# Performance work log

Hardware: AMD Instinct MI355X
Metric: run time of the kernel (lower is better)

Reference implementation:

```python
import jax, jax.numpy as jnp
import numpy as np

N_NODES = 100000
N_EDGES = 1600000
N_GRAPHS = 128
D = 64
EPS = 1e-5


def layer_norm(h, gamma, beta):
    mu = jnp.mean(h, axis=-1, keepdims=True)
    var = jnp.var(h, axis=-1, keepdims=True)
    return (h - mu) * jax.lax.rsqrt(var + EPS) * gamma + beta


def setup_inputs() -> dict:
    key = jax.random.key(0)
    ks = jax.random.split(key, 9)
    x = jax.random.normal(ks[0], (N_NODES, D), dtype=jnp.float32)
    edge_index = jax.random.randint(ks[1], (2, N_EDGES), 0, N_NODES, dtype=jnp.int64)
    batch = jnp.sort(jax.random.randint(ks[2], (N_NODES,), 0, N_GRAPHS, dtype=jnp.int64))
    graph_embed = jax.random.normal(ks[3], (N_GRAPHS, D), dtype=jnp.float32)
    s = 1.0 / np.sqrt(D)
    W_self = jax.random.uniform(ks[4], (D, D), jnp.float32, -s, s)
    W_neigh = jax.random.uniform(ks[5], (D, D), jnp.float32, -s, s)
    b = jax.random.uniform(ks[6], (D,), jnp.float32, -s, s)
    gamma = jnp.ones((D,), jnp.float32)
    beta = jnp.zeros((D,), jnp.float32)
    return {"x": x, "edge_index": edge_index, "batch": batch,
            "graph_embed": graph_embed, "W_self": W_self, "W_neigh": W_neigh,
            "b": b, "gamma": gamma, "beta": beta}


def reference(x, edge_index, batch, graph_embed, W_self, W_neigh, b, gamma, beta):
    src, dst = edge_index[0], edge_index[1]
    # mean neighbor aggregation: gather src features, scatter-add into dst
    msg_sum = jax.ops.segment_sum(x[src], dst, num_segments=N_NODES)  # [N, D]
    deg = jax.ops.segment_sum(jnp.ones((N_EDGES,), x.dtype), dst, num_segments=N_NODES)
    h_neigh = msg_sum / jnp.maximum(deg, 1.0)[:, None]
    # SAGEConv combine
    node_out = x @ W_self + h_neigh @ W_neigh + b  # [N, D]
    # graph_aggr='add' pooling over batch assignment
    graph_out = jax.ops.segment_sum(node_out, batch, num_segments=N_GRAPHS)  # [G, D]
    # residual (channel_match=True -> no projection)
    node_out = node_out + x
    graph_out = graph_out + graph_embed
    # norm then act; note: original applies norm TWICE to graph_out and no ReLU on it
    node_out = jax.nn.relu(layer_norm(node_out, gamma, beta))
    graph_out = layer_norm(layer_norm(graph_out, gamma, beta), gamma, beta)
    return (node_out, graph_out)
```

## Files before the change

kernel.cpp:

```cpp
#include <hip/hip_runtime.h>

#define N_NODES  100000
#define N_EDGES  1600000
#define N_GRAPHS 128
#define DD       64
#define EPSV     1e-5f

#define BSH      5
#define BMASK    31
#define NBUCK    3125
#define NBPAD    4096
#define CAPB     768

#define THRP     1024
#define EPT      16
#define BLKE     (THRP*EPT)
#define NBLK     ((N_EDGES + BLKE - 1) / BLKE)

#define O_ORD   200704u
#define O_DESC  6754304u
#define O_GACC  9801216u
#define O_XB    9834496u
#define O_WTF   22634496u
#define WS_NEED (O_WTF + 16384u)

typedef __attribute__((ext_vector_type(8))) short bf16x8;
typedef __attribute__((ext_vector_type(4))) float f32x4;
typedef __attribute__((ext_vector_type(2))) float f32x2;

__device__ __forceinline__ ushort bf16rne(float f) {
  uint u = __float_as_uint(f);
  return (ushort)((u + 0x7FFFu + ((u >> 16) & 1u)) >> 16);
}
__device__ __forceinline__ uint pk2(float lo, float hi) {
  return (uint)bf16rne(lo) | ((uint)bf16rne(hi) << 16);
}

__global__ __launch_bounds__(256) void cast_k(const float* __restrict__ x, ushort* __restrict__ xb,
                                              float* __restrict__ gacc) {
  int i = blockIdx.x * 256 + threadIdx.x;
  if (i < N_GRAPHS * DD) gacc[i] = 0.f;
  if (i < 128) gacc[N_GRAPHS * DD + i] = 0.f;
  float4 v = ((const float4*)x)[i];
  uint4 u = *(const uint4*)&v;
  ushort4 o;
  o.x = (ushort)((u.x + 0x7FFFu + ((u.x >> 16) & 1)) >> 16);
  o.y = (ushort)((u.y + 0x7FFFu + ((u.y >> 16) & 1)) >> 16);
  o.z = (ushort)((u.z + 0x7FFFu + ((u.z >> 16) & 1)) >> 16);
  o.w = (ushort)((u.w + 0x7FFFu + ((u.w >> 16) & 1)) >> 16);
  ((ushort4*)xb)[i] = o;
}

__global__ __launch_bounds__(1024) void scatS_k(const int* __restrict__ ei,
                                                int* __restrict__ ordered,
                                                int* __restrict__ desc,
                                                const float* __restrict__ Wself,
                                                const float* __restrict__ Wneigh,
                                                ushort* __restrict__ wtf) {
  __shared__ int hist[NBPAD];
  __shared__ int cur2[NBPAD];
  __shared__ int wtot[16];
  int t = threadIdx.x;
  if (blockIdx.x == 0) {
    int lane = t & 63, ks = (t >> 6) & 3, tile = (t >> 8) & 1, nt = t >> 9;
    int brow = (nt << 5) + (tile << 4) + (lane & 15);
    int k0 = (ks << 5) + (((lane >> 4) & 3) << 3);
    uint4 o;
    uint p[4];
#pragma unroll
    for (int jj = 0; jj < 4; ++jj) {
      int k = k0 + jj * 2;
      float w0 = (k < 64)     ? Wself[k * DD + brow]       : Wneigh[(k - 64) * DD + brow];
      float w1 = (k + 1 < 64) ? Wself[(k + 1) * DD + brow] : Wneigh[(k - 63) * DD + brow];
      p[jj] = pk2(w0, w1);
    }
    o.x = p[0]; o.y = p[1]; o.z = p[2]; o.w = p[3];
    ((uint4*)wtf)[t] = o;
  }
  for (int i = t; i < NBPAD; i += THRP) hist[i] = 0;
  __syncthreads();
  int e0 = blockIdx.x * BLKE;
  int pk[EPT], bn[EPT];
#pragma unroll
  for (int j = 0; j < EPT; ++j) {
    int e = e0 + j * THRP + t;
    bn[j] = -1;
    if (e < N_EDGES) {
      int s = ei[e], d = ei[N_EDGES + e];
      bn[j] = d >> BSH;
      pk[j] = s | ((d & BMASK) << 17);
      atomicAdd(&hist[bn[j]], 1);
    }
  }
  __syncthreads();
  int h0 = hist[4 * t], h1 = hist[4 * t + 1], h2 = hist[4 * t + 2], h3 = hist[4 * t + 3];
  int s = h0 + h1 + h2 + h3;
  int lane = t & 63, wv = t >> 6;
  int inc = s;
#pragma unroll
  for (int off = 1; off < 64; off <<= 1) {
    int u = __shfl_up(inc, off);
    if (lane >= off) inc += u;
  }
  if (lane == 63) wtot[wv] = inc;
  __syncthreads();
  if (t < 16) {
    int v = wtot[t];
    int iv = v;
#pragma unroll
    for (int off = 1; off < 16; off <<= 1) {
      int u = __shfl_up(iv, off);
      if (t >= off) iv += u;
    }
    wtot[t] = iv - v;
  }
  __syncthreads();
  int base = wtot[wv] + (inc - s);
  cur2[4 * t]     = base;
  cur2[4 * t + 1] = base + h0;
  cur2[4 * t + 2] = base + h0 + h1;
  cur2[4 * t + 3] = base + h0 + h1 + h2;
  {
    int dbase = blockIdx.x * NBUCK;
#pragma unroll
    for (int i = 0; i < 4; ++i) {
      int bb = 4 * t + i;
      if (bb < NBUCK) desc[dbase + bb] = (cur2[bb] << 10) | hist[bb];
    }
  }
  __syncthreads();
  int obase = blockIdx.x * BLKE;
#pragma unroll
  for (int j = 0; j < EPT; ++j) {
    if (bn[j] >= 0) {
      int sp = atomicAdd(&cur2[bn[j]], 1);
      ordered[obase + sp] = pk[j];
    }
  }
}

__global__ __launch_bounds__(256, 8) void aggM_k(const ushort* __restrict__ xb,
                                                 const int* __restrict__ ordered,
                                                 const int* __restrict__ desc,
                                                 const ushort* __restrict__ wtf,
                                                 const float* __restrict__ bvec,
                                                 const float* __restrict__ gamma,
                                                 const float* __restrict__ beta,
                                                 const int* __restrict__ batch,
                                                 float* __restrict__ gacc,
                                                 float* __restrict__ out) {
  __shared__ short As[32 * 128];
  __shared__ float Cbuf[32 * 65];
  __shared__ int sorted[CAPB + 16];
  __shared__ int hist[32], startc[32], curl[32];
  __shared__ int wsum2[2];
  __shared__ int nTot_s;
  int* slabL = (int*)Cbuf;
  int t = threadIdx.x;
  int b = blockIdx.x;
  int node0 = b << BSH;
  if (t < 32) hist[t] = 0;
  {
    uint4 v = ((const uint4*)(xb + (size_t)node0 * DD))[t];
    uint r = (uint)t >> 3, c = (uint)t & 7;
    *(uint4*)((char*)As + r * 256u + ((c * 16u) ^ ((r & 7u) << 4))) = v;
  }
  int dsc = (t < NBLK) ? desc[t * NBUCK + b] : 0;
  int c   = dsc & 1023;
  int st  = dsc >> 10;
  int inc = c;
  if (t < 128) {
    int lane = t & 63;
#pragma unroll
    for (int off = 1; off < 64; off <<= 1) {
      int u = __shfl_up(inc, off);
      if (lane >= off) inc += u;
    }
    if (lane == 63) wsum2[t >> 6] = inc;
  }
  __syncthreads();
  int pos = 0;
  if (t < 128) pos = ((t >> 6) ? wsum2[0] : 0) + inc - c;
  if (t == 0) nTot_s = wsum2[0] + wsum2[1];
  if (t < NBLK) {
    int lim = CAPB - pos;
    int cc = c < lim ? c : (lim > 0 ? lim : 0);
    const int* srcp = ordered + (size_t)t * BLKE + st;
    for (int i = 0; i < cc; ++i) slabL[pos + i] = srcp[i];
  }
  __syncthreads();
  int n = nTot_s;
  if (n > CAPB) n = CAPB;
  int w0 = -1, w1 = -1, w2 = -1;
  if (t < n)       { w0 = slabL[t];       atomicAdd(&hist[w0 >> 17], 1); }
  if (t + 256 < n) { w1 = slabL[t + 256]; atomicAdd(&hist[w1 >> 17], 1); }
  if (t + 512 < n) { w2 = slabL[t + 512]; atomicAdd(&hist[w2 >> 17], 1); }
  __syncthreads();
  if (t < 32) {
    int h = hist[t];
    int v = h;
#pragma unroll
    for (int off = 1; off < 32; off <<= 1) {
      int u = __shfl_up(v, off);
      if (t >= off) v += u;
    }
    startc[t] = v - h;
    curl[t]   = v - h;
  }
  __syncthreads();
  if (w0 >= 0) { int p = atomicAdd(&curl[w0 >> 17], 1); sorted[p] = ((w0 & 0x1FFFF) << 7) + 512; }
  if (w1 >= 0) { int p = atomicAdd(&curl[w1 >> 17], 1); sorted[p] = ((w1 & 0x1FFFF) << 7) + 512; }
  if (w2 >= 0) { int p = atomicAdd(&curl[w2 >> 17], 1); sorted[p] = ((w2 & 0x1FFFF) << 7) + 512; }
  __syncthreads();
  int wl   = __builtin_amdgcn_readfirstlane(t >> 6);
  int lane = t & 63;
  int g    = lane >> 4;
  int sub  = lane & 15;
  const char* zb = (const char*)xb - 512;
  uint subb = (uint)sub * 8u;
  for (int r = wl; r < 32; r += 4) {
    int s0 = startc[r], dg = hist[r];
    f32x2 A01 = {0.f, 0.f}, A23 = {0.f, 0.f};
    for (int j = 0; j < dg; j += 16) {
      int e0 = j + g, e1 = j + 4 + g, e2 = j + 8 + g, e3 = j + 12 + g;
      uint o0 = (uint)sorted[s0 + e0]; if (e0 >= dg) o0 = 0u;
      uint o1 = (uint)sorted[s0 + e1]; if (e1 >= dg) o1 = 0u;
      uint o2 = (uint)sorted[s0 + e2]; if (e2 >= dg) o2 = 0u;
      uint o3 = (uint)sorted[s0 + e3]; if (e3 >= dg) o3 = 0u;
      uint2 u0 = *(const uint2*)(zb + o0 + subb);
      uint2 u1 = *(const uint2*)(zb + o1 + subb);
      uint2 u2 = *(const uint2*)(zb + o2 + subb);
      uint2 u3 = *(const uint2*)(zb + o3 + subb);
      f32x2 v0, v1, v2, v3, y0, y1, y2, y3;
      v0.x = __uint_as_float(u0.x << 16); v0.y = __uint_as_float(u0.x & 0xFFFF0000u);
      v1.x = __uint_as_float(u1.x << 16); v1.y = __uint_as_float(u1.x & 0xFFFF0000u);
      v2.x = __uint_as_float(u2.x << 16); v2.y = __uint_as_float(u2.x & 0xFFFF0000u);
      v3.x = __uint_as_float(u3.x << 16); v3.y = __uint_as_float(u3.x & 0xFFFF0000u);
      y0.x = __uint_as_float(u0.y << 16); y0.y = __uint_as_float(u0.y & 0xFFFF0000u);
      y1.x = __uint_as_float(u1.y << 16); y1.y = __uint_as_float(u1.y & 0xFFFF0000u);
      y2.x = __uint_as_float(u2.y << 16); y2.y = __uint_as_float(u2.y & 0xFFFF0000u);
      y3.x = __uint_as_float(u3.y << 16); y3.y = __uint_as_float(u3.y & 0xFFFF0000u);
      A01 += (v0 + v1) + (v2 + v3);
      A23 += (y0 + y1) + (y2 + y3);
    }
    float a0 = A01.x, a1 = A01.y, a2 = A23.x, a3 = A23.y;
#pragma unroll
    for (int off = 16; off <= 32; off <<= 1) {
      a0 += __shfl_xor(a0, off);
      a1 += __shfl_xor(a1, off);
      a2 += __shfl_xor(a2, off);
      a3 += __shfl_xor(a3, off);
    }
    if (g == 0) {
      float inv = 1.f / fmaxf((float)dg, 1.f);
      uint2 pw;
      pw.x = pk2(a0 * inv, a1 * inv);
      pw.y = pk2(a2 * inv, a3 * inv);
      uint rr = (uint)r;
      *(uint2*)((char*)As + rr * 256u + ((128u + (uint)sub * 8u) ^ ((rr & 7u) << 4))) = pw;
    }
  }
  __syncthreads();
  f32x4 acc0 = {0.f, 0.f, 0.f, 0.f}, acc1 = {0.f, 0.f, 0.f, 0.f};
  uint mrow  = (uint)(wl >> 1) << 4;
  int  nt    = wl & 1;
  uint arow  = mrow + (uint)(lane & 15);
  uint kc    = ((uint)(lane >> 4)) * 16u;
#pragma unroll 1
  for (int ks = 0; ks < 4; ++ks) {
    uint kb = (uint)ks * 64u + kc;
    bf16x8 af = *(const bf16x8*)((const char*)As + arow * 256u + (kb ^ ((arow & 7u) << 4)));
    bf16x8 b0 = *(const bf16x8*)(wtf + (size_t)(((nt * 2 + 0) * 4 + ks) * 64 + lane) * 8);
    bf16x8 b1 = *(const bf16x8*)(wtf + (size_t)(((nt * 2 + 1) * 4 + ks) * 64 + lane) * 8);
    acc0 = __builtin_amdgcn_mfma_f32_16x16x32_bf16(af, b0, acc0, 0, 0, 0);
    acc1 = __builtin_amdgcn_mfma_f32_16x16x32_bf16(af, b1, acc1, 0, 0, 0);
  }
  {
    uint nbase = (uint)nt << 5;
    uint rr = mrow + (((uint)(lane >> 4)) << 2);
    uint cc = nbase + (uint)(lane & 15);
#pragma unroll
    for (int j = 0; j < 4; ++j) {
      uint rj = rr + (uint)j;
      Cbuf[rj * 65u + cc]       = acc0[j];
      Cbuf[rj * 65u + cc + 16u] = acc1[j];
    }
  }
  __syncthreads();
  float bv  = bvec[lane];
  float gv  = gamma[lane];
  float btv = beta[lane];
  int r0 = wl * 8;
  int gprev = -1; float pool = 0.f;
#pragma unroll
  for (int m = 0; m < 8; ++m) {
    uint r = (uint)(r0 + m);
    int node = node0 + r0 + m;
    float cval = Cbuf[r * 65u + (uint)lane];
    float tmp = cval + bv;
    int gi = batch[node];
    if (gi != gprev) {
      if (gprev >= 0) atomicAdd(&gacc[gprev * DD + lane], pool);
      pool = 0.f; gprev = gi;
    }
    pool += tmp;
    ushort xv16 = *(const ushort*)((const char*)As + r * 256u + (((uint)lane * 2u) ^ ((r & 7u) << 4)));
    float val = tmp + __uint_as_float((uint)xv16 << 16);
    float s = val;
    for (int off = 32; off; off >>= 1) s += __shfl_xor(s, off);
    float mu  = s * (1.f / 64.f);
    float dlt = val - mu;
    float ss  = dlt * dlt;
    for (int off = 32; off; off >>= 1) ss += __shfl_xor(ss, off);
    float rstd = rsqrtf(ss * (1.f / 64.f) + EPSV);
    float o = dlt * rstd * gv + btv;
    out[(size_t)node * DD + lane] = fmaxf(o, 0.f);
  }
  if (gprev >= 0) atomicAdd(&gacc[gprev * DD + lane], pool);
}

__global__ __launch_bounds__(256) void graph_k(const float* __restrict__ gacc, const float* __restrict__ gemb,
                                               const float* __restrict__ gamma, const float* __restrict__ beta,
                                               float* __restrict__ out) {
  int lane = threadIdx.x & 63;
  int w = blockIdx.x * 4 + (threadIdx.x >> 6);
  if (w >= N_GRAPHS) return;
  float v = gacc[w * DD + lane] + gemb[w * DD + lane];
  float gv = gamma[lane], btv = beta[lane];
#pragma unroll
  for (int it = 0; it < 2; ++it) {
    float s = v;
    for (int off = 32; off; off >>= 1) s += __shfl_xor(s, off);
    float mu  = s * (1.f / 64.f);
    float d   = v - mu;
    float ss  = d * d;
    for (int off = 32; off; off >>= 1) ss += __shfl_xor(ss, off);
    v = d * rsqrtf(ss * (1.f / 64.f) + EPSV) * gv + btv;
  }
  out[(size_t)N_NODES * DD + w * DD + lane] = v;
}

extern "C" void kernel_launch(void* const* d_in, const int* in_sizes, int n_in,
                              void* d_out, int out_size, void* d_ws, size_t ws_size,
                              hipStream_t stream) {
  const float* x      = (const float*)d_in[0];
  const int*   ei     = (const int*)d_in[1];
  const int*   batch  = (const int*)d_in[2];
  const float* gemb   = (const float*)d_in[3];
  const float* Wself  = (const float*)d_in[4];
  const float* Wneigh = (const float*)d_in[5];
  const float* bvec   = (const float*)d_in[6];
  const float* gamma  = (const float*)d_in[7];
  const float* beta   = (const float*)d_in[8];

  char* ws = (char*)d_ws;
  int*    ordered = (int*)(ws + O_ORD);
  int*    desc    = (int*)(ws + O_DESC);
  float*  gacc    = (float*)(ws + O_GACC);
  ushort* xb      = (ushort*)(ws + O_XB);
  ushort* wtf     = (ushort*)(ws + O_WTF);
  float*  outf    = (float*)d_out;

  cast_k <<<N_NODES * DD / 4 / 256, 256, 0, stream>>>(x, xb, gacc);
  scatS_k<<<NBLK, THRP, 0, stream>>>(ei, ordered, desc, Wself, Wneigh, wtf);
  aggM_k <<<NBUCK, 256, 0, stream>>>(xb, ordered, desc, wtf, bvec, gamma, beta,
                                     batch, gacc, outf);
  graph_k<<<N_GRAPHS / 4, 256, 0, stream>>>(gacc, gemb, gamma, beta, outf);
}
```

Baseline: 89.40 us.

## Transpose bucket descriptors and gather edges by binary search instead of serial copy

After: 87.45 us. 1.02x faster.

```diff
diff --git a/kernel.cpp b/kernel.cpp
--- a/kernel.cpp
+++ b/kernel.cpp
@@ -121,11 +121,10 @@
   cur2[4 * t + 2] = base + h0 + h1;
   cur2[4 * t + 3] = base + h0 + h1 + h2;
   {
-    int dbase = blockIdx.x * NBUCK;
 #pragma unroll
     for (int i = 0; i < 4; ++i) {
       int bb = 4 * t + i;
-      if (bb < NBUCK) desc[dbase + bb] = (cur2[bb] << 10) | hist[bb];
+      if (bb < NBUCK) desc[bb * NBLK + blockIdx.x] = (cur2[bb] << 10) | hist[bb];
     }
   }
   __syncthreads();
@@ -155,7 +154,8 @@
   __shared__ int hist[32], startc[32], curl[32];
   __shared__ int wsum2[2];
   __shared__ int nTot_s;
-  int* slabL = (int*)Cbuf;
+  int* posA = sorted;
+  int* stA  = sorted + 128;
   int t = threadIdx.x;
   int b = blockIdx.x;
   int node0 = b << BSH;
@@ -165,7 +165,7 @@
     uint r = (uint)t >> 3, c = (uint)t & 7;
     *(uint4*)((char*)As + r * 256u + ((c * 16u) ^ ((r & 7u) << 4))) = v;
   }
-  int dsc = (t < NBLK) ? desc[t * NBUCK + b] : 0;
+  int dsc = (t < NBLK) ? desc[b * NBLK + t] : 0;
   int c   = dsc & 1023;
   int st  = dsc >> 10;
   int inc = c;
@@ -179,22 +179,28 @@
     if (lane == 63) wsum2[t >> 6] = inc;
   }
   __syncthreads();
-  int pos = 0;
-  if (t < 128) pos = ((t >> 6) ? wsum2[0] : 0) + inc - c;
+  if (t < 128) {
+    int pos = ((t >> 6) ? wsum2[0] : 0) + inc - c;
+    posA[t] = (t < NBLK) ? pos : 0x7FFFFFFF;
+    stA[t]  = t * BLKE + st;
+  }
   if (t == 0) nTot_s = wsum2[0] + wsum2[1];
-  if (t < NBLK) {
-    int lim = CAPB - pos;
-    int cc = c < lim ? c : (lim > 0 ? lim : 0);
-    const int* srcp = ordered + (size_t)t * BLKE + st;
-    for (int i = 0; i < cc; ++i) slabL[pos + i] = srcp[i];
-  }
   __syncthreads();
   int n = nTot_s;
   if (n > CAPB) n = CAPB;
+  auto bs_load = [&](int i) -> int {
+    int lo = 0;
+#pragma unroll
+    for (int stp = 64; stp; stp >>= 1) {
+      int cnd = lo + stp;
+      lo = (posA[cnd] <= i) ? cnd : lo;
+    }
+    return ordered[stA[lo] + (i - posA[lo])];
+  };
   int w0 = -1, w1 = -1, w2 = -1;
-  if (t < n)       { w0 = slabL[t];       atomicAdd(&hist[w0 >> 17], 1); }
-  if (t + 256 < n) { w1 = slabL[t + 256]; atomicAdd(&hist[w1 >> 17], 1); }
-  if (t + 512 < n) { w2 = slabL[t + 512]; atomicAdd(&hist[w2 >> 17], 1); }
+  if (t < n)       { w0 = bs_load(t);       atomicAdd(&hist[w0 >> 17], 1); }
+  if (t + 256 < n) { w1 = bs_load(t + 256); atomicAdd(&hist[w1 >> 17], 1); }
+  if (t + 512 < n) { w2 = bs_load(t + 512); atomicAdd(&hist[w2 >> 17], 1); }
   __syncthreads();
   if (t < 32) {
     int h = hist[t];
```
